# Kernel tuning notes

Hardware: AMD Instinct MI355X
Metric: run time of the kernel (lower is better)

The kernel has to match this reference:

```python
import jax, jax.numpy as jnp
import numpy as np

B, D, N = 4, 96, 512
ATTN = 256
OUT = 1


def setup_inputs() -> dict:
    key = jax.random.key(0)
    ks = jax.random.split(key, 4)
    x = jax.random.normal(ks[0], (B, D, N), dtype=jnp.float32)
    Wg1 = jax.random.normal(ks[1], (ATTN, D), dtype=jnp.float32) / np.sqrt(D)
    Wg2 = jax.random.normal(ks[2], (ATTN, D), dtype=jnp.float32) / np.sqrt(D)
    bg = jnp.zeros((ATTN,), dtype=jnp.float32)
    Wa_w = jax.random.normal(ks[3], (OUT, ATTN), dtype=jnp.float32) / np.sqrt(ATTN)
    Wa_b = jnp.zeros((OUT,), dtype=jnp.float32)
    ba = jnp.zeros((OUT,), dtype=jnp.float32)
    return {"x": x, "Wg1": Wg1, "Wg2": Wg2, "bg": bg, "Wa_w": Wa_w, "Wa_b": Wa_b, "ba": ba}


def reference(x, Wg1, Wg2, bg, Wa_w, Wa_b, ba):
    # x: (B, D, N) -> transpose to (B, N, D)
    xt = jnp.swapaxes(x, 1, 2)
    g1 = jnp.einsum("bnd,ad->bna", xt, Wg1)  # (B, N, ATTN)
    g2 = jnp.einsum("bnd,ad->bna", xt, Wg2)  # (B, N, ATTN)
    # pairwise additive scores: (B, N, N, ATTN)
    gnn = jnp.tanh(g1[:, :, None, :] + g2[:, None, :, :] + bg)
    # project to scalar per pair, add both biases (Wa bias and ba), sigmoid
    att = jax.nn.sigmoid(jnp.einsum("bnma,oa->bnmo", gnn, Wa_w) + Wa_b + ba)
    att = att.squeeze(-1)  # (B, N, N)
    return jnp.matmul(att, xt)  # (B, N, D)
```

## Files before the change

kernel.cpp:

```cpp
#include <hip/hip_runtime.h>
#include <math.h>

#define NB 4
#define ND 96
#define NN 512
#define NA 256

static constexpr float C_TANH = 2.8853900817779268f;
static constexpr float LOG2E  = 1.4426950408889634f;

__device__ __forceinline__ float fexp2(float x) {
#if __has_builtin(__builtin_amdgcn_exp2f)
  return __builtin_amdgcn_exp2f(x);
#else
  return exp2f(x);
#endif
}
__device__ __forceinline__ float frcp(float x) {
#if __has_builtin(__builtin_amdgcn_rcpf)
  return __builtin_amdgcn_rcpf(x);
#else
  return 1.0f / x;
#endif
}

__global__ __launch_bounds__(256) void k_wt(const float* __restrict__ Wg1,
                                            const float* __restrict__ Wg2,
                                            float* __restrict__ W1t,
                                            float* __restrict__ W2t) {
  int idx = blockIdx.x * 256 + threadIdx.x;
  int mat = idx / (ND * NA);
  int rem = idx - mat * (ND * NA);
  int d = rem >> 8;
  int a = rem & 255;
  const float* s = mat ? Wg2 : Wg1;
  float* t = mat ? W2t : W1t;
  t[d * NA + a] = s[a * ND + d];
}

__global__ __launch_bounds__(256) void k_s0(const float* __restrict__ Wa_w,
                                            const float* __restrict__ Wa_b,
                                            const float* __restrict__ ba,
                                            float* __restrict__ S0) {
  __shared__ float red[256];
  int t = threadIdx.x;
  red[t] = Wa_w[t];
  __syncthreads();
  for (int s = 128; s > 0; s >>= 1) {
    if (t < s) red[t] += red[t + s];
    __syncthreads();
  }
  if (t == 0) S0[0] = red[0] + Wa_b[0] + ba[0];
}

__global__ __launch_bounds__(256) void k_proj(const float* __restrict__ x,
                                              const float* __restrict__ W1t,
                                              const float* __restrict__ W2t,
                                              const float* __restrict__ bg,
                                              float* __restrict__ G1,
                                              float* __restrict__ G2,
                                              float* __restrict__ xt) {
  __shared__ float xsh[8][ND];
  const int tid = threadIdx.x;
  const int b = blockIdx.x >> 6;
  const int n0 = (blockIdx.x & 63) * 8;

  for (int idx = tid; idx < 8 * ND; idx += 256) {
    int d = idx >> 3, j = idx & 7;
    float v = x[(size_t)(b * ND + d) * NN + n0 + j];
    xsh[j][d] = v;
    xt[(size_t)(b * NN + n0 + j) * ND + d] = v;
  }
  __syncthreads();

  const int a = tid;
  float acc1[8], acc2[8];
  float bgv = bg[a];
#pragma unroll
  for (int j = 0; j < 8; ++j) { acc1[j] = bgv; acc2[j] = 0.f; }

  for (int d = 0; d < ND; ++d) {
    float w1 = W1t[d * NA + a];
    float w2 = W2t[d * NA + a];
#pragma unroll
    for (int j = 0; j < 8; ++j) {
      float xv = xsh[j][d];
      acc1[j] = fmaf(w1, xv, acc1[j]);
      acc2[j] = fmaf(w2, xv, acc2[j]);
    }
  }
#pragma unroll
  for (int j = 0; j < 8; ++j) {
    G1[(size_t)(b * NN + n0 + j) * NA + a] = C_TANH * acc1[j];
    G2[(size_t)(b * NN + n0 + j) * NA + a] = C_TANH * acc2[j];
  }
}

__global__ __launch_bounds__(256, 2) void k_main(const float* __restrict__ G1,
                                                 const float* __restrict__ G2,
                                                 const float* __restrict__ xt,
                                                 const float* __restrict__ Wa_w,
                                                 const float* __restrict__ S0p,
                                                 float* __restrict__ out) {
  __shared__ float4 g2sh[4096];
  __shared__ float attsh[4][NN];
  const int tid = threadIdx.x;
  const int b = blockIdx.x >> 7;
  const int n0 = (blockIdx.x & 127) << 2;
  const float S0 = S0p[0];
  const float4* __restrict__ W4 = (const float4*)Wa_w;
  const float* __restrict__ g1r0 = G1 + (size_t)(b * NN + n0) * NA;

  for (int p = 0; p < 2; ++p) {
    float acc[4] = {0.f, 0.f, 0.f, 0.f};
    const float4* __restrict__ srcbase = (const float4*)(G2 + (size_t)(b * NN + p * 256) * NA);
    for (int c = 0; c < 4; ++c) {
      __syncthreads();
      const float4* __restrict__ src = srcbase + c * 16;
#pragma unroll
      for (int k = 0; k < 16; ++k) {
        int f = k * 256 + tid;
        int r = f >> 4;
        int q = f & 15;
        g2sh[r * 16 + (q ^ (r & 7))] = src[r * 64 + q];
      }
      __syncthreads();
      const int a0 = c * 64;
#pragma unroll
      for (int k4 = 0; k4 < 16; ++k4) {
        float4 v = g2sh[tid * 16 + (k4 ^ (tid & 7))];
        float g2v[4] = {v.x, v.y, v.z, v.w};
        float4 wq = W4[(a0 >> 2) + k4];
        float wv[4] = {wq.x, wq.y, wq.z, wq.w};
        float g1v[4][4];
#pragma unroll
        for (int nl = 0; nl < 4; ++nl) {
          float4 g = *(const float4*)(g1r0 + nl * NA + a0 + k4 * 4);
          g1v[nl][0] = g.x; g1v[nl][1] = g.y; g1v[nl][2] = g.z; g1v[nl][3] = g.w;
        }
#pragma unroll
        for (int j = 0; j < 4; ++j) {
#pragma unroll
          for (int nl = 0; nl < 4; ++nl) {
            float e = fexp2(g1v[nl][j] + g2v[j]);
            acc[nl] = fmaf(wv[j], frcp(1.f + e), acc[nl]);
          }
        }
      }
    }
#pragma unroll
    for (int nl = 0; nl < 4; ++nl) {
      float z = S0 - 2.f * acc[nl];
      attsh[nl][p * 256 + tid] = frcp(1.f + fexp2(-LOG2E * z));
    }
  }
  __syncthreads();

  const int w = tid >> 6;
  const int l = tid & 63;
  const float* __restrict__ xb = xt + (size_t)b * NN * ND;
  const float* __restrict__ arow = attsh[w];
  float o0 = 0.f, o1 = 0.f;
  for (int m = 0; m < NN; ++m) {
    float av = arow[m];
    const float* xr = xb + m * ND;
    o0 = fmaf(av, xr[l], o0);
    o1 = fmaf(av, xr[64 + (l & 31)], o1);
  }
  float* orow = out + (size_t)(b * NN + n0 + w) * ND;
  orow[l] = o0;
  if (l < 32) orow[64 + l] = o1;
}

extern "C" void kernel_launch(void* const* d_in, const int* in_sizes, int n_in,
                              void* d_out, int out_size, void* d_ws, size_t ws_size,
                              hipStream_t stream) {
  const float* x    = (const float*)d_in[0];
  const float* Wg1  = (const float*)d_in[1];
  const float* Wg2  = (const float*)d_in[2];
  const float* bg   = (const float*)d_in[3];
  const float* Wa_w = (const float*)d_in[4];
  const float* Wa_b = (const float*)d_in[5];
  const float* ba   = (const float*)d_in[6];
  float* out = (float*)d_out;

  float* ws  = (float*)d_ws;
  float* G1  = ws;
  float* G2  = ws + 524288;
  float* xtw = ws + 1048576;
  float* W1t = ws + 1245184;
  float* W2t = ws + 1269760;
  float* S0  = ws + 1294336;

  hipLaunchKernelGGL(k_wt,   dim3(192), dim3(256), 0, stream, Wg1, Wg2, W1t, W2t);
  hipLaunchKernelGGL(k_s0,   dim3(1),   dim3(256), 0, stream, Wa_w, Wa_b, ba, S0);
  hipLaunchKernelGGL(k_proj, dim3(256), dim3(256), 0, stream, x, W1t, W2t, bg, G1, G2, xtw);
  hipLaunchKernelGGL(k_main, dim3(512), dim3(256), 0, stream, G1, G2, xtw, Wa_w, S0, out);
}
```

Measured before the change: 195.7 us.

## Chunk G2 by attention slice, shrink main-kernel LDS, merge prep kernels

The projection kernel now writes G2 in a chunked layout of 32-wide attention slices per batch, so each k_main stage loads a contiguous block. This halves the per-stage shared-memory tile and raises the launch-bounds occupancy hint from 2 to 4 blocks per CU. The weight-transpose and bias-sum kernels are merged into one launch, and the projection uses 4 rows per block over twice as many blocks. In exchange there are more synchronisation stages per pass, and the higher occupancy target may limit registers.

Result: faster. 169.8 us (-13.2%).

```diff
diff --git a/kernel.cpp b/kernel.cpp
--- a/kernel.cpp
+++ b/kernel.cpp
@@ -24,85 +24,93 @@
 #endif
 }
 
-__global__ __launch_bounds__(256) void k_wt(const float* __restrict__ Wg1,
-                                            const float* __restrict__ Wg2,
-                                            float* __restrict__ W1t,
-                                            float* __restrict__ W2t) {
+__global__ __launch_bounds__(256) void k_prep(const float* __restrict__ Wg1,
+                                              const float* __restrict__ Wg2,
+                                              const float* __restrict__ Wa_w,
+                                              const float* __restrict__ Wa_b,
+                                              const float* __restrict__ ba,
+                                              float* __restrict__ W1t,
+                                              float* __restrict__ W2t,
+                                              float* __restrict__ S0) {
+  if (blockIdx.x == 192) {
+    __shared__ float red[256];
+    int t = threadIdx.x;
+    red[t] = Wa_w[t];
+    __syncthreads();
+    for (int s = 128; s > 0; s >>= 1) {
+      if (t < s) red[t] += red[t + s];
+      __syncthreads();
+    }
+    if (t == 0) S0[0] = red[0] + Wa_b[0] + ba[0];
+    return;
+  }
   int idx = blockIdx.x * 256 + threadIdx.x;
   int mat = idx / (ND * NA);
   int rem = idx - mat * (ND * NA);
   int d = rem >> 8;
   int a = rem & 255;
-  const float* s = mat ? Wg2 : Wg1;
-  float* t = mat ? W2t : W1t;
-  t[d * NA + a] = s[a * ND + d];
-}
-
-__global__ __launch_bounds__(256) void k_s0(const float* __restrict__ Wa_w,
-                                            const float* __restrict__ Wa_b,
-                                            const float* __restrict__ ba,
-                                            float* __restrict__ S0) {
-  __shared__ float red[256];
-  int t = threadIdx.x;
-  red[t] = Wa_w[t];
+  (mat ? W2t : W1t)[d * NA + a] = (mat ? Wg2 : Wg1)[a * ND + d];
+}
+
+__global__ __launch_bounds__(256, 2) void k_proj(const float* __restrict__ x,
+                                                 const float* __restrict__ W1t,
+                                                 const float* __restrict__ W2t,
+                                                 const float* __restrict__ bg,
+                                                 float* __restrict__ G1,
+                                                 float* __restrict__ G2c,
+                                                 float* __restrict__ xt) {
+  __shared__ float4 xsh[ND];
+  const int tid = threadIdx.x;
+  const int b = blockIdx.x >> 7;
+  const int n0 = (blockIdx.x & 127) * 4;
+
+  for (int idx = tid; idx < ND * 4; idx += 256) {
+    int d = idx >> 2, j = idx & 3;
+    float v = x[(size_t)(b * ND + d) * NN + n0 + j];
+    ((float*)&xsh[d])[j] = v;
+    xt[(size_t)(b * NN + n0 + j) * ND + d] = v;
+  }
   __syncthreads();
-  for (int s = 128; s > 0; s >>= 1) {
-    if (t < s) red[t] += red[t + s];
-    __syncthreads();
-  }
-  if (t == 0) S0[0] = red[0] + Wa_b[0] + ba[0];
-}
-
-__global__ __launch_bounds__(256) void k_proj(const float* __restrict__ x,
-                                              const float* __restrict__ W1t,
-                                              const float* __restrict__ W2t,
-                                              const float* __restrict__ bg,
-                                              float* __restrict__ G1,
-                                              float* __restrict__ G2,
-                                              float* __restrict__ xt) {
-  __shared__ float xsh[8][ND];
-  const int tid = threadIdx.x;
-  const int b = blockIdx.x >> 6;
-  const int n0 = (blockIdx.x & 63) * 8;
-
-  for (int idx = tid; idx < 8 * ND; idx += 256) {
-    int d = idx >> 3, j = idx & 7;
-    float v = x[(size_t)(b * ND + d) * NN + n0 + j];
-    xsh[j][d] = v;
-    xt[(size_t)(b * NN + n0 + j) * ND + d] = v;
-  }
-  __syncthreads();
 
   const int a = tid;
-  float acc1[8], acc2[8];
-  float bgv = bg[a];
-#pragma unroll
-  for (int j = 0; j < 8; ++j) { acc1[j] = bgv; acc2[j] = 0.f; }
-
-  for (int d = 0; d < ND; ++d) {
-    float w1 = W1t[d * NA + a];
-    float w2 = W2t[d * NA + a];
-#pragma unroll
-    for (int j = 0; j < 8; ++j) {
-      float xv = xsh[j][d];
-      acc1[j] = fmaf(w1, xv, acc1[j]);
-      acc2[j] = fmaf(w2, xv, acc2[j]);
-    }
-  }
-#pragma unroll
-  for (int j = 0; j < 8; ++j) {
+  const float bgv = bg[a];
+  float acc1[4], acc2[4];
+#pragma unroll
+  for (int j = 0; j < 4; ++j) { acc1[j] = bgv; acc2[j] = 0.f; }
+
+  for (int d4 = 0; d4 < ND / 4; ++d4) {
+    float w1[4], w2[4];
+#pragma unroll
+    for (int dd = 0; dd < 4; ++dd) {
+      w1[dd] = W1t[(d4 * 4 + dd) * NA + a];
+      w2[dd] = W2t[(d4 * 4 + dd) * NA + a];
+    }
+#pragma unroll
+    for (int dd = 0; dd < 4; ++dd) {
+      float4 xq = xsh[d4 * 4 + dd];
+      float xv[4] = {xq.x, xq.y, xq.z, xq.w};
+#pragma unroll
+      for (int j = 0; j < 4; ++j) {
+        acc1[j] = fmaf(w1[dd], xv[j], acc1[j]);
+        acc2[j] = fmaf(w2[dd], xv[j], acc2[j]);
+      }
+    }
+  }
+  const int c = a >> 5, al = a & 31;
+#pragma unroll
+  for (int j = 0; j < 4; ++j) {
     G1[(size_t)(b * NN + n0 + j) * NA + a] = C_TANH * acc1[j];
-    G2[(size_t)(b * NN + n0 + j) * NA + a] = C_TANH * acc2[j];
-  }
-}
-
-__global__ __launch_bounds__(256, 2) void k_main(const float* __restrict__ G1,
-                                                 const float* __restrict__ G2,
+    G2c[((size_t)(b * 8 + c) * NN + n0 + j) * 32 + al] = C_TANH * acc2[j];
+  }
+}
+
+__global__ __launch_bounds__(256, 4) void k_main(const float* __restrict__ G1,
+                                                 const float* __restrict__ G2c,
                                                  const float* __restrict__ xt,
                                                  const float* __restrict__ Wa_w,
                                                  const float* __restrict__ S0p,
                                                  float* __restrict__ out) {
-  __shared__ float4 g2sh[4096];
+  __shared__ float4 g2sh[256 * 8];
   __shared__ float attsh[4][NN];
   const int tid = threadIdx.x;
   const int b = blockIdx.x >> 7;
@@ -113,36 +121,30 @@
 
   for (int p = 0; p < 2; ++p) {
     float acc[4] = {0.f, 0.f, 0.f, 0.f};
-    const float4* __restrict__ srcbase = (const float4*)(G2 + (size_t)(b * NN + p * 256) * NA);
-    for (int c = 0; c < 4; ++c) {
+    for (int c = 0; c < 8; ++c) {
+      const float4* __restrict__ src =
+          (const float4*)(G2c + ((size_t)(b * 8 + c) * NN + p * 256) * 32);
       __syncthreads();
-      const float4* __restrict__ src = srcbase + c * 16;
-#pragma unroll
-      for (int k = 0; k < 16; ++k) {
+#pragma unroll
+      for (int k = 0; k < 8; ++k) {
         int f = k * 256 + tid;
-        int r = f >> 4;
-        int q = f & 15;
-        g2sh[r * 16 + (q ^ (r & 7))] = src[r * 64 + q];
+        int r = f >> 3, q = f & 7;
+        g2sh[r * 8 + (q ^ (r & 7))] = src[f];
       }
       __syncthreads();
-      const int a0 = c * 64;
-#pragma unroll
-      for (int k4 = 0; k4 < 16; ++k4) {
-        float4 v = g2sh[tid * 16 + (k4 ^ (tid & 7))];
+#pragma unroll
+      for (int k4 = 0; k4 < 8; ++k4) {
+        float4 v = g2sh[tid * 8 + (k4 ^ (tid & 7))];
         float g2v[4] = {v.x, v.y, v.z, v.w};
-        float4 wq = W4[(a0 >> 2) + k4];
+        float4 wq = W4[c * 8 + k4];
         float wv[4] = {wq.x, wq.y, wq.z, wq.w};
-        float g1v[4][4];
 #pragma unroll
         for (int nl = 0; nl < 4; ++nl) {
-          float4 g = *(const float4*)(g1r0 + nl * NA + a0 + k4 * 4);
-          g1v[nl][0] = g.x; g1v[nl][1] = g.y; g1v[nl][2] = g.z; g1v[nl][3] = g.w;
-        }
-#pragma unroll
-        for (int j = 0; j < 4; ++j) {
-#pragma unroll
-          for (int nl = 0; nl < 4; ++nl) {
-            float e = fexp2(g1v[nl][j] + g2v[j]);
+          float4 g = *(const float4*)(g1r0 + nl * NA + c * 32 + k4 * 4);
+          float g1v[4] = {g.x, g.y, g.z, g.w};
+#pragma unroll
+          for (int j = 0; j < 4; ++j) {
+            float e = fexp2(g1v[j] + g2v[j]);
             acc[nl] = fmaf(wv[j], frcp(1.f + e), acc[nl]);
           }
         }
@@ -186,14 +188,16 @@
 
   float* ws  = (float*)d_ws;
   float* G1  = ws;
-  float* G2  = ws + 524288;
+  float* G2c = ws + 524288;
   float* xtw = ws + 1048576;
   float* W1t = ws + 1245184;
   float* W2t = ws + 1269760;
   float* S0  = ws + 1294336;
 
-  hipLaunchKernelGGL(k_wt,   dim3(192), dim3(256), 0, stream, Wg1, Wg2, W1t, W2t);
-  hipLaunchKernelGGL(k_s0,   dim3(1),   dim3(256), 0, stream, Wa_w, Wa_b, ba, S0);
-  hipLaunchKernelGGL(k_proj, dim3(256), dim3(256), 0, stream, x, W1t, W2t, bg, G1, G2, xtw);
-  hipLaunchKernelGGL(k_main, dim3(512), dim3(256), 0, stream, G1, G2, xtw, Wa_w, S0, out);
-}
+  hipLaunchKernelGGL(k_prep, dim3(193), dim3(256), 0, stream,
+                     Wg1, Wg2, Wa_w, Wa_b, ba, W1t, W2t, S0);
+  hipLaunchKernelGGL(k_proj, dim3(512), dim3(256), 0, stream,
+                     x, W1t, W2t, bg, G1, G2c, xtw);
+  hipLaunchKernelGGL(k_main, dim3(512), dim3(256), 0, stream,
+                     G1, G2c, xtw, Wa_w, S0, out);
+}
```
